# Kernel optimization log

Hardware: AMD Instinct MI355X
Metric: run time of the kernel (lower is better)

## Reference

```python
import jax, jax.numpy as jnp
import numpy as np

B, T, C = 4, 2048, 768
H, D = 12, 64          # num_heads, head_size
R = 64                 # kv_lora_rank
ROPE_THETA = 10000.0


def setup_inputs() -> dict:
    key = jax.random.key(0)
    ks = jax.random.split(key, 8)
    s = lambda fan_in: 1.0 / np.sqrt(fan_in)
    return {
        "x":      jax.random.normal(ks[0], (B, T, C), jnp.float32),
        "Wq":     jax.random.normal(ks[1], (C, H * D), jnp.float32) * s(C),
        "Wdown":  jax.random.normal(ks[2], (C, R), jnp.float32) * s(C),
        "ln_g":   jnp.ones((R,), jnp.float32),
        "ln_b":   jnp.zeros((R,), jnp.float32),
        "Wup":    jax.random.normal(ks[3], (R, 2 * H * D), jnp.float32) * s(R),
        "Wo":     jax.random.normal(ks[4], (H * D, C), jnp.float32) * s(H * D),
        "bo":     jnp.zeros((C,), jnp.float32),
    }


def _rope_cos_sin(t, d, dtype):
    # freqs over half-dim, repeated twice (rotate-half convention)
    inv_freq = 1.0 / (ROPE_THETA ** (jnp.arange(0, d, 2, dtype=jnp.float32) / d))
    ang = jnp.arange(t, dtype=jnp.float32)[:, None] * inv_freq[None, :]  # [T, D/2]
    ang = jnp.concatenate([ang, ang], axis=-1)                            # [T, D]
    return jnp.cos(ang).astype(dtype), jnp.sin(ang).astype(dtype)


def _apply_rope(q, cos, sin):
    # q: [B, H, T, D]; cos/sin: [T, D]
    d2 = q.shape[-1] // 2
    rot = jnp.concatenate([-q[..., d2:], q[..., :d2]], axis=-1)
    return q * cos + rot * sin


def reference(x, Wq, Wdown, ln_g, ln_b, Wup, Wo, bo):
    b, t, c = x.shape
    q = (x @ Wq).reshape(b, t, H, D).transpose(0, 2, 1, 3)  # [B,H,T,D]

    ckv = x @ Wdown                                         # [B,T,R]
    mu = jnp.mean(ckv, axis=-1, keepdims=True)
    var = jnp.var(ckv, axis=-1, keepdims=True)
    ckv = (ckv - mu) * jax.lax.rsqrt(var + 1e-5) * ln_g + ln_b

    kv = (ckv @ Wup).reshape(b, t, 2, H, D)
    k = kv[:, :, 0].transpose(0, 2, 1, 3)                   # [B,H,T,D]
    v = kv[:, :, 1].transpose(0, 2, 1, 3)

    cos, sin = _rope_cos_sin(t, D, x.dtype)
    q = _apply_rope(q, cos, sin)
    k = _apply_rope(k, cos, sin)

    wei = jnp.einsum("bhqd,bhkd->bhqk", q, k) * (D ** -0.5)
    causal = jnp.tril(jnp.ones((t, t), bool))
    wei = jnp.where(causal, wei, -jnp.inf)
    wei = jax.nn.softmax(wei, axis=-1)                      # dropout: eval mode (identity)

    out = jnp.einsum("bhqk,bhkd->bhqd", wei, v)             # [B,H,T,D]
    out = out.transpose(0, 2, 1, 3).reshape(b, t, H * D)
    return out @ Wo + bo
```

## Files before the change

### kernel.cpp

```cpp
#include <hip/hip_runtime.h>
#include <hip/hip_bf16.h>
#include <math.h>

#define B_ 4
#define T_ 2048
#define C_ 768
#define H_ 12
#define D_ 64
#define R_ 64
#define BT_ (B_*T_)
#define HD_ (H_*D_)

typedef __attribute__((ext_vector_type(8))) short bf16x8;
typedef __attribute__((ext_vector_type(4))) float f32x4;
typedef __attribute__((ext_vector_type(16))) float f32x16;

__device__ inline short f2bf(float f) {
  union { float f; unsigned u; } x; x.f = f;
  unsigned r = x.u + 0x7fffu + ((x.u >> 16) & 1u);
  return (short)(r >> 16);
}
__device__ inline unsigned pk_bf16(float a, float b) {
#if __has_builtin(__builtin_amdgcn_cvt_pk_bf16_f32)
  auto t = __builtin_amdgcn_cvt_pk_bf16_f32(a, b);
  unsigned u; __builtin_memcpy(&u, &t, sizeof(unsigned)); return u;
#else
  union { float f; unsigned u; } x, y; x.f = a; y.f = b;
  unsigned ra = (x.u + 0x7fffu + ((x.u >> 16) & 1u)) >> 16;
  unsigned rb = (y.u + 0x7fffu + ((y.u >> 16) & 1u)) & 0xffff0000u;
  return ra | rb;
#endif
}
__device__ inline float fexp2(float x) {
#if __has_builtin(__builtin_amdgcn_exp2f)
  return __builtin_amdgcn_exp2f(x);
#else
  return exp2f(x);
#endif
}
__device__ inline void pswap(unsigned &a, unsigned &b) {
#if __has_builtin(__builtin_amdgcn_permlane32_swap)
  auto r = __builtin_amdgcn_permlane32_swap((int)a, (int)b, false, false);
  unsigned u[2]; __builtin_memcpy(u, &r, 8);
  a = u[0]; b = u[1];
#else
  unsigned ax = __shfl_xor(a, 32), bx = __shfl_xor(b, 32);
  bool hi = (threadIdx.x & 32) != 0;
  unsigned na = hi ? bx : a;
  unsigned nb = hi ? b : ax;
  a = na; b = nb;
#endif
}
typedef __attribute__((address_space(3))) unsigned lds_u32;
typedef __attribute__((address_space(1))) const unsigned glb_u32;
__device__ inline void gload_lds16(const void* g, void* l) {
  __builtin_amdgcn_global_load_lds((glb_u32*)g, (lds_u32*)l, 16, 0, 0);
}

#define SC2_ 0.18033688f

__device__ __attribute__((always_inline)) inline void ttile(
    const float* __restrict__ src, short* __restrict__ dst,
    int Kd, int Ns, int k0, int n0, int tid, float (*tl)[33]) {
  int tx = tid & 31, ty = tid >> 5;
  #pragma unroll
  for (int r = 0; r < 4; ++r)
    tl[ty + 8 * r][tx] = src[(size_t)(k0 + ty + 8 * r) * Ns + n0 + tx];
  __syncthreads();
  #pragma unroll
  for (int r = 0; r < 4; ++r)
    dst[(size_t)(n0 + ty + 8 * r) * Kd + k0 + tx] = f2bf(tl[tx][ty + 8 * r]);
}

__global__ __launch_bounds__(256) void prep_conv(
    const float* __restrict__ Wq, const float* __restrict__ Wd,
    const float* __restrict__ Wup, const float* __restrict__ Wo,
    short* __restrict__ W1T, short* __restrict__ WupT, short* __restrict__ WvoT,
    float* __restrict__ cs, float* __restrict__ sn) {
  __shared__ float SH[32 * 65 + 64 * 33];
  float (*tl)[33] = (float(*)[33])SH;
  int tid = threadIdx.x, blk = blockIdx.x;
  if (blk < 576) {
    int tk = blk % 24, tn = blk / 24;
    ttile(Wq, W1T, 768, 768, tk * 32, tn * 32, tid, tl);
  } else if (blk < 624) {
    int l = blk - 576; int tk = l % 24, tn = l / 24;
    ttile(Wd, W1T + (size_t)768 * 768, 768, 64, tk * 32, tn * 32, tid, tl);
  } else if (blk < 672) {
    int l = blk - 624; int tk = l % 2, tn = l / 2;
    ttile(Wup, WupT, 64, 1536, tk * 32, tn * 32, tid, tl);
  } else if (blk < 1248) {
    int l = blk - 672;
    int h = l / 48, rem = l % 48, tc = rem >> 1, tr = rem & 1;
    float* a  = SH;
    float* bm = SH + 32 * 65;
    #pragma unroll
    for (int i = 0; i < 8; ++i) {
      int idx = tid + i * 256;
      int r = idx >> 6, d = idx & 63;
      a[r * 65 + d] = Wup[(size_t)(tr * 32 + r) * 1536 + 768 + h * 64 + d];
      int dd = idx >> 5, c = idx & 31;
      bm[dd * 33 + c] = Wo[(size_t)(h * 64 + dd) * 768 + tc * 32 + c];
    }
    __syncthreads();
    int r = tid & 31, cj = tid >> 5;
    float s0 = 0.f, s1 = 0.f, s2 = 0.f, s3 = 0.f;
    #pragma unroll
    for (int d = 0; d < 64; ++d) {
      float av = a[r * 65 + d];
      const float* bp = &bm[d * 33 + cj * 4];
      s0 += av * bp[0]; s1 += av * bp[1]; s2 += av * bp[2]; s3 += av * bp[3];
    }
    int colb = tc * 32 + cj * 4;
    size_t krow = (size_t)(h * 64 + tr * 32 + r);
    WvoT[(size_t)(colb + 0) * 768 + krow] = f2bf(s0);
    WvoT[(size_t)(colb + 1) * 768 + krow] = f2bf(s1);
    WvoT[(size_t)(colb + 2) * 768 + krow] = f2bf(s2);
    WvoT[(size_t)(colb + 3) * 768 + krow] = f2bf(s3);
  } else {
    int base = (blk - 1248) * 1024;
    #pragma unroll
    for (int i = 0; i < 4; ++i) {
      int idx = base + tid + i * 256;
      int j = idx & 31, t = idx >> 5;
      float invf = exp2f(-(float)j * (13.287712379549449f / 32.f));
      float ang = (float)t * invf;
      cs[idx] = cosf(ang);
      sn[idx] = sinf(ang);
    }
  }
}

__global__ __launch_bounds__(256) void gemm0_k(
    const float* __restrict__ Af, const short* __restrict__ Bt,
    const float* __restrict__ bias, const float* __restrict__ bias2,
    short* __restrict__ ob0, short* __restrict__ ob1, short* __restrict__ obT,
    const float* __restrict__ cs, const float* __restrict__ sn)
{
  constexpr int K = 768;
  __shared__ short SM[2 * 16384];
  const int m0 = blockIdx.x * 128;
  const int n0 = blockIdx.y * 128;
  const int tid = threadIdx.x, lane = tid & 63, w = tid >> 6;
  const int wr = w >> 1, wc = w & 1;
  const int fr = lane & 15, fk = (lane >> 4) * 8;
  const int rstage = lane >> 3, cstage = (lane & 7) * 8;

  f32x4 acc[4][4] = {};
  auto As = [&](int buf) -> short* { return SM + buf * 16384; };
  auto Bs = [&](int buf) -> short* { return SM + buf * 16384 + 8192; };

  auto compute = [&](const short* Asb, const short* Bsb) {
    #pragma unroll
    for (int kk = 0; kk < 64; kk += 32) {
      bf16x8 a[4], b[4];
      #pragma unroll
      for (int mi = 0; mi < 4; ++mi)
        a[mi] = *(const bf16x8*)&Asb[(wr * 64 + mi * 16 + fr) * 64 + kk + fk];
      #pragma unroll
      for (int ni = 0; ni < 4; ++ni)
        b[ni] = *(const bf16x8*)&Bsb[(wc * 64 + ni * 16 + fr) * 64 + kk + fk];
      #pragma unroll
      for (int mi = 0; mi < 4; ++mi)
        #pragma unroll
        for (int ni = 0; ni < 4; ++ni)
          acc[mi][ni] = __builtin_amdgcn_mfma_f32_16x16x32_bf16(a[mi], b[ni], acc[mi][ni], 0, 0, 0);
    }
  };
  auto stageB = [&](short* Bsb, int k0) {
    #pragma unroll
    for (int i = 0; i < 4; ++i) {
      int c = w * 4 + i;
      int r = c * 8 + rstage;
      gload_lds16(&Bt[(size_t)(n0 + r) * K + k0 + cstage], Bsb + c * 512);
    }
  };

  float4 fa[8];
  auto loadA = [&](int k0) {
    #pragma unroll
    for (int i = 0; i < 4; ++i) {
      int idx = tid + 256 * i;
      int row = idx >> 3, c8 = idx & 7;
      const float* src = Af + (size_t)(m0 + row) * 768 + k0 + c8 * 8;
      fa[2 * i]     = *(const float4*)(src);
      fa[2 * i + 1] = *(const float4*)(src + 4);
    }
  };
  auto writeA = [&](short* Asb) {
    #pragma unroll
    for (int i = 0; i < 4; ++i) {
      int idx = tid + 256 * i;
      int row = idx >> 3, c8 = idx & 7;
      uint4 uu;
      uu.x = pk_bf16(fa[2 * i].x,     fa[2 * i].y);
      uu.y = pk_bf16(fa[2 * i].z,     fa[2 * i].w);
      uu.z = pk_bf16(fa[2 * i + 1].x, fa[2 * i + 1].y);
      uu.w = pk_bf16(fa[2 * i + 1].z, fa[2 * i + 1].w);
      *(uint4*)&Asb[row * 64 + c8 * 8] = uu;
    }
  };

  loadA(0);
  stageB(Bs(0), 0);
  writeA(As(0));
  __syncthreads();

  int buf = 0;
  for (int k0 = 0; k0 < K; k0 += 64) {
    bool nxt = (k0 + 64 < K);
    if (nxt) { loadA(k0 + 64); stageB(Bs(buf ^ 1), k0 + 64); }
    compute(As(buf), Bs(buf));
    if (nxt) writeA(As(buf ^ 1));
    __syncthreads();
    buf ^= 1;
  }

  const int er = (lane >> 4) * 4, ec = lane & 15;
  const int cb = n0 + wc * 64;

  if (cb < 768) {
    int h = cb >> 6;
    #pragma unroll
    for (int mi = 0; mi < 4; ++mi)
      #pragma unroll
      for (int r = 0; r < 4; ++r) {
        int row = m0 + wr * 64 + mi * 16 + er + r;
        int t = row & (T_ - 1), bb = row >> 11;
        short* dst = ob0 + (((size_t)(bb * H_ + h)) * T_ + t) * 64;
        #pragma unroll
        for (int ni = 0; ni < 2; ++ni) {
          int d = ni * 16 + ec;
          float c = cs[t * 32 + d] * SC2_, s = sn[t * 32 + d] * SC2_;
          float x0 = acc[mi][ni][r], x1 = acc[mi][ni + 2][r];
          dst[d]      = f2bf(x0 * c - x1 * s);
          dst[d + 32] = f2bf(x1 * c + x0 * s);
        }
      }
  } else if (cb == 768) {
    short* Wl = SM + w * 2560;
    int bb = m0 >> 11;
    int dl = lane >> 2, tlo = (lane & 3) * 8;
    #pragma unroll
    for (int hp = 0; hp < 2; ++hp) {
      #pragma unroll
      for (int mi2 = 0; mi2 < 2; ++mi2) {
        int mi = hp * 2 + mi2;
        short vb[4][4];
        #pragma unroll
        for (int r = 0; r < 4; ++r) {
          float s = 0.f, s2 = 0.f;
          #pragma unroll
          for (int ni = 0; ni < 4; ++ni) { float v = acc[mi][ni][r]; s += v; s2 += v * v; }
          #pragma unroll
          for (int off = 1; off < 16; off <<= 1) {
            s  += __shfl_xor(s, off);
            s2 += __shfl_xor(s2, off);
          }
          float mu = s * (1.f / 64.f);
          float var = s2 * (1.f / 64.f) - mu * mu;
          float rstd = rsqrtf(var + 1e-5f);
          int row = m0 + wr * 64 + mi * 16 + er + r;
          #pragma unroll
          for (int ni = 0; ni < 4; ++ni) {
            int d = ni * 16 + ec;
            short q = f2bf((acc[mi][ni][r] - mu) * rstd * bias[d] + bias2[d]);
            vb[r][ni] = q;
            ob1[(size_t)row * 64 + d] = q;
          }
        }
        int tl0 = mi2 * 16 + er;
        #pragma unroll
        for (int ni = 0; ni < 4; ++ni) {
          int d = ni * 16 + ec;
          uint2 uu;
          uu.x = (unsigned)(unsigned short)vb[0][ni] | ((unsigned)(unsigned short)vb[1][ni] << 16);
          uu.y = (unsigned)(unsigned short)vb[2][ni] | ((unsigned)(unsigned short)vb[3][ni] << 16);
          *(uint2*)&Wl[d * 40 + tl0] = uu;
        }
      }
      int tg0 = (m0 & (T_ - 1)) + wr * 64 + hp * 32;
      #pragma unroll
      for (int j = 0; j < 4; ++j) {
        int d = j * 16 + dl;
        uint4 vv = *(const uint4*)&Wl[d * 40 + tlo];
        *(uint4*)&obT[((size_t)(bb * 64 + d)) * T_ + tg0 + tlo] = vv;
      }
    }
  }
}

__global__ __launch_bounds__(256) void gemm1_k(
    const short* __restrict__ A, const short* __restrict__ Bt,
    short* __restrict__ ob0,
    const float* __restrict__ cs, const float* __restrict__ sn)
{
  constexpr int K = 64;
  __shared__ short SM[2 * 8192];
  short* As = SM;
  short* Bs = SM + 8192;
  const int m0 = blockIdx.x * 128;
  const int n0 = blockIdx.y * 128;
  const int tid = threadIdx.x, lane = tid & 63, w = tid >> 6;
  const int wr = w >> 1, wc = w & 1;
  const int fr = lane & 15, fk = (lane >> 4) * 8;
  const int rstage = lane >> 3, cstage = (lane & 7) * 8;

  f32x4 acc[4][4] = {};

  #pragma unroll
  for (int i = 0; i < 4; ++i) {
    int c = w * 4 + i;
    int r = c * 8 + rstage;
    gload_lds16(&A[(size_t)(m0 + r) * K + cstage], As + c * 512);
    gload_lds16(&Bt[(size_t)(n0 + r) * K + cstage], Bs + c * 512);
  }
  __syncthreads();
  #pragma unroll
  for (int kk = 0; kk < 64; kk += 32) {
    bf16x8 a[4], b[4];
    #pragma unroll
    for (int mi = 0; mi < 4; ++mi)
      a[mi] = *(const bf16x8*)&As[(wr * 64 + mi * 16 + fr) * 64 + kk + fk];
    #pragma unroll
    for (int ni = 0; ni < 4; ++ni)
      b[ni] = *(const bf16x8*)&Bs[(wc * 64 + ni * 16 + fr) * 64 + kk + fk];
    #pragma unroll
    for (int mi = 0; mi < 4; ++mi)
      #pragma unroll
      for (int ni = 0; ni < 4; ++ni)
        acc[mi][ni] = __builtin_amdgcn_mfma_f32_16x16x32_bf16(a[mi], b[ni], acc[mi][ni], 0, 0, 0);
  }

  const int er = (lane >> 4) * 4, ec = lane & 15;
  const int cb = n0 + wc * 64;
  int h = cb >> 6;
  #pragma unroll
  for (int mi = 0; mi < 4; ++mi)
    #pragma unroll
    for (int r = 0; r < 4; ++r) {
      int row = m0 + wr * 64 + mi * 16 + er + r;
      int t = row & (T_ - 1), bb = row >> 11;
      short* dst = ob0 + (((size_t)(bb * H_ + h)) * T_ + t) * 64;
      #pragma unroll
      for (int ni = 0; ni < 2; ++ni) {
        int d = ni * 16 + ec;
        float c = cs[t * 32 + d], s = sn[t * 32 + d];
        float x0 = acc[mi][ni][r], x1 = acc[mi][ni + 2][r];
        dst[d]      = f2bf(x0 * c - x1 * s);
        dst[d + 32] = f2bf(x1 * c + x0 * s);
      }
    }
}

__global__ __launch_bounds__(256) void attn_mfma(
    const short* __restrict__ qgl, const short* __restrict__ kg,
    const short* __restrict__ vtg, short* __restrict__ o)
{
  __shared__ short SMa[2][2][8 * 512];

  const int bh = blockIdx.x;
  const int u  = 15 - blockIdx.y;
  const int tid = threadIdx.x, lane = tid & 63, w = tid >> 6;
  const int q32 = lane & 31, half = lane >> 5;
  const int b = bh / H_, h = bh - b * H_;
  const short* kb  = kg  + (size_t)bh * T_ * 64;
  const short* vtb = vtg + (size_t)b * 64 * T_;

  const int wq = 4 * u + w;
  const int q0 = wq * 32;
  const int last_w = (wq >> 1) * 64;
  const int qidx = q0 + q32;
  const int kend = (2 * u + 1) * 64;

  const short* qrow = qgl + ((size_t)bh * T_ + qidx) * 64;
  bf16x8 bq[4];
  #pragma unroll
  for (int ks = 0; ks < 4; ++ks)
    bq[ks] = *(const bf16x8*)&qrow[ks * 16 + half * 8];

  f32x16 oacc[2] = {};
  float lrun = 0.f;

  auto stage = [&](int buf, int kt) {
    #pragma unroll
    for (int i = 0; i < 2; ++i) {
      int c = w * 2 + i;
      int kh = c >> 2, ks = c & 3;
      gload_lds16(kb + (size_t)(kt + kh * 32 + q32) * 64 + ks * 16 + half * 8,
                  &SMa[buf][0][c * 512]);
      gload_lds16(vtb + (size_t)(kh * 32 + q32) * T_ + kt + ks * 16 + half * 8,
                  &SMa[buf][1][c * 512]);
    }
  };

  stage(0, 0);
  __syncthreads();

  int cur = 0;
  for (int kt = 0; kt <= kend; kt += 64) {
    if (kt + 64 <= kend) stage(cur ^ 1, kt + 64);

    if (kt <= last_w) {
      const short* Kc = &SMa[cur][0][0];
      const short* Vc = &SMa[cur][1][0];
      const bool diag = (kt == last_w);
      const int dkh = diag ? (wq & 1) : 2;
      const bool skip1 = diag && ((wq & 1) == 0);

      bf16x8 bp[4];
      #pragma unroll
      for (int kh = 0; kh < 2; ++kh) {
        if (kh == 1 && skip1) break;
        f32x16 sacc = {};
        __builtin_amdgcn_s_setprio(1);
        #pragma unroll
        for (int ks = 0; ks < 4; ++ks) {
          bf16x8 a = *(const bf16x8*)&Kc[(kh * 4 + ks) * 512 + lane * 8];
          sacc = __builtin_amdgcn_mfma_f32_32x32x16_bf16(a, bq[ks], sacc, 0, 0, 0);
        }
        __builtin_amdgcn_s_setprio(0);
        float pv[16];
        if (kh != dkh) {
          #pragma unroll
          for (int r = 0; r < 16; ++r) pv[r] = fexp2(sacc[r]);
        } else {
          #pragma unroll
          for (int r = 0; r < 16; ++r) {
            int key = kt + kh * 32 + (r & 3) + 8 * (r >> 2) + 4 * half;
            pv[r] = (key <= qidx) ? fexp2(sacc[r]) : 0.f;
          }
        }
        float t0 = (pv[0] + pv[1]) + (pv[2] + pv[3]);
        float t1 = (pv[4] + pv[5]) + (pv[6] + pv[7]);
        float t2 = (pv[8] + pv[9]) + (pv[10] + pv[11]);
        float t3 = (pv[12] + pv[13]) + (pv[14] + pv[15]);
        lrun += (t0 + t1) + (t2 + t3);
        unsigned l0 = pk_bf16(pv[0],  pv[1]),  h0 = pk_bf16(pv[2],  pv[3]);
        unsigned l1 = pk_bf16(pv[4],  pv[5]),  h1 = pk_bf16(pv[6],  pv[7]);
        unsigned l2 = pk_bf16(pv[8],  pv[9]),  h2 = pk_bf16(pv[10], pv[11]);
        unsigned l3 = pk_bf16(pv[12], pv[13]), h3 = pk_bf16(pv[14], pv[15]);
        pswap(l0, l1); pswap(h0, h1);
        pswap(l2, l3); pswap(h2, h3);
        union { unsigned u[4]; bf16x8 v; } f0, f1;
        f0.u[0] = l0; f0.u[1] = h0; f0.u[2] = l1; f0.u[3] = h1;
        f1.u[0] = l2; f1.u[1] = h2; f1.u[2] = l3; f1.u[3] = h3;
        bp[2 * kh + 0] = f0.v;
        bp[2 * kh + 1] = f1.v;
      }

      __builtin_amdgcn_s_setprio(1);
      #pragma unroll
      for (int ks = 0; ks < 2; ++ks)
        #pragma unroll
        for (int dt = 0; dt < 2; ++dt) {
          bf16x8 av = *(const bf16x8*)&Vc[(dt * 4 + ks) * 512 + lane * 8];
          oacc[dt] = __builtin_amdgcn_mfma_f32_32x32x16_bf16(av, bp[ks], oacc[dt], 0, 0, 0);
        }
      if (!skip1) {
        #pragma unroll
        for (int ks = 2; ks < 4; ++ks)
          #pragma unroll
          for (int dt = 0; dt < 2; ++dt) {
            bf16x8 av = *(const bf16x8*)&Vc[(dt * 4 + ks) * 512 + lane * 8];
            oacc[dt] = __builtin_amdgcn_mfma_f32_32x32x16_bf16(av, bp[ks], oacc[dt], 0, 0, 0);
          }
      }
      __builtin_amdgcn_s_setprio(0);
    }

    __syncthreads();
    cur ^= 1;
  }

  float ltot = lrun + __shfl_xor(lrun, 32);
  float inv = 1.f / ltot;
  short* Pw = &SMa[0][0][0] + w * 2304;
  #pragma unroll
  for (int dt = 0; dt < 2; ++dt)
    #pragma unroll
    for (int g2 = 0; g2 < 4; ++g2) {
      uint2 uu;
      uu.x = pk_bf16(oacc[dt][4 * g2 + 0] * inv, oacc[dt][4 * g2 + 1] * inv);
      uu.y = pk_bf16(oacc[dt][4 * g2 + 2] * inv, oacc[dt][4 * g2 + 3] * inv);
      *(uint2*)&Pw[q32 * 72 + dt * 32 + 8 * g2 + 4 * half] = uu;
    }
  int row = lane >> 1, seg = lane & 1;
  int t = q0 + row;
  short* orow = o + ((size_t)(b * T_ + t)) * HD_ + h * 64 + seg * 32;
  #pragma unroll
  for (int i = 0; i < 4; ++i) {
    uint4 vv = *(const uint4*)&Pw[row * 72 + seg * 32 + i * 8];
    *(uint4*)&orow[i * 8] = vv;
  }
}

__global__ __launch_bounds__(256) void gemm_out(
    const short* __restrict__ A, const short* __restrict__ Bt,
    float* __restrict__ out0, const float* __restrict__ bias)
{
  constexpr int K = HD_, N = C_;
  __shared__ short SM[2 * (8192 + 4096)];
  const int m0 = blockIdx.x * 128;
  const int n0 = blockIdx.y * 64;
  const int tid = threadIdx.x, lane = tid & 63, w = tid >> 6;
  const int fr = lane & 15, fk = (lane >> 4) * 8;
  const int rstage = lane >> 3, cstage = (lane & 7) * 8;

  f32x4 acc[2][4] = {};

  auto As = [&](int buf) -> short* { return SM + buf * 12288; };
  auto Bs = [&](int buf) -> short* { return SM + buf * 12288 + 8192; };

  auto stage = [&](int buf, int k0) {
    #pragma unroll
    for (int i = 0; i < 4; ++i) {
      int c = w * 4 + i;
      int r = c * 8 + rstage;
      gload_lds16(&A[(size_t)(m0 + r) * K + k0 + cstage], As(buf) + c * 512);
    }
    #pragma unroll
    for (int i = 0; i < 2; ++i) {
      int c = w * 2 + i;
      int r = c * 8 + rstage;
      gload_lds16(&Bt[(size_t)(n0 + r) * K + k0 + cstage], Bs(buf) + c * 512);
    }
  };

  stage(0, 0);
  __syncthreads();

  int buf = 0;
  for (int k0 = 0; k0 < K; k0 += 64) {
    if (k0 + 64 < K) stage(buf ^ 1, k0 + 64);
    #pragma unroll
    for (int kk = 0; kk < 64; kk += 32) {
      bf16x8 a[2], b[4];
      a[0] = *(const bf16x8*)&As(buf)[(w * 32 +      fr) * 64 + kk + fk];
      a[1] = *(const bf16x8*)&As(buf)[(w * 32 + 16 + fr) * 64 + kk + fk];
      #pragma unroll
      for (int ni = 0; ni < 4; ++ni)
        b[ni] = *(const bf16x8*)&Bs(buf)[(ni * 16 + fr) * 64 + kk + fk];
      #pragma unroll
      for (int mi = 0; mi < 2; ++mi)
        #pragma unroll
        for (int ni = 0; ni < 4; ++ni)
          acc[mi][ni] = __builtin_amdgcn_mfma_f32_16x16x32_bf16(a[mi], b[ni], acc[mi][ni], 0, 0, 0);
    }
    __syncthreads();
    buf ^= 1;
  }

  const int er = (lane >> 4) * 4, ec = lane & 15;
  #pragma unroll
  for (int mi = 0; mi < 2; ++mi)
    #pragma unroll
    for (int r = 0; r < 4; ++r) {
      int row = m0 + w * 32 + mi * 16 + er + r;
      #pragma unroll
      for (int ni = 0; ni < 4; ++ni) {
        int col = n0 + ni * 16 + ec;
        out0[(size_t)row * N + col] = acc[mi][ni][r] + bias[col];
      }
    }
}

extern "C" void kernel_launch(void* const* d_in, const int* in_sizes, int n_in,
                              void* d_out, int out_size, void* d_ws, size_t ws_size,
                              hipStream_t stream) {
  (void)in_sizes; (void)n_in; (void)out_size; (void)ws_size;
  const float* x     = (const float*)d_in[0];
  const float* Wq    = (const float*)d_in[1];
  const float* Wdown = (const float*)d_in[2];
  const float* ln_g  = (const float*)d_in[3];
  const float* ln_b  = (const float*)d_in[4];
  const float* Wup   = (const float*)d_in[5];
  const float* Wo    = (const float*)d_in[6];
  const float* bo    = (const float*)d_in[7];
  float* out = (float*)d_out;

  char* w = (char*)d_ws;
  short* W1T    = (short*)w;  w += (size_t)896 * C_    * 2;
  short* WupT   = (short*)w;  w += (size_t)HD_ * R_    * 2;
  short* WvoT   = (short*)w;  w += (size_t)C_ * HD_    * 2;
  short* ckv    = (short*)w;  w += (size_t)BT_ * R_    * 2;
  short* ckvT   = (short*)w;  w += (size_t)B_ * R_ * T_ * 2;
  short* qb     = (short*)w;  w += (size_t)BT_ * HD_   * 2;
  short* kb     = (short*)w;  w += (size_t)BT_ * HD_   * 2;
  short* att    = (short*)w;  w += (size_t)BT_ * HD_   * 2;
  float* cs_t   = (float*)w;  w += (size_t)T_ * 32 * 4;
  float* sn_t   = (float*)w;  w += (size_t)T_ * 32 * 4;

  prep_conv<<<1312, 256, 0, stream>>>(Wq, Wdown, Wup, Wo,
                                      W1T, WupT, WvoT, cs_t, sn_t);

  gemm0_k<<<dim3(BT_/128, 7), 256, 0, stream>>>(
      x, W1T, ln_g, ln_b, qb, ckv, ckvT, cs_t, sn_t);

  gemm1_k<<<dim3(BT_/128, 6), 256, 0, stream>>>(
      ckv, WupT, kb, cs_t, sn_t);

  attn_mfma<<<dim3(B_*H_, 16), 256, 0, stream>>>(qb, kb, ckvT, att);

  gemm_out<<<dim3(BT_/128, 12), 256, 0, stream>>>(att, WvoT, out, bo);
}
```

Measured before the change: 195.7 us.

## Fuse K up-projection with RoPE into latent-panel blocks of first GEMM

Removes the separate gemm1 kernel. The blocks that compute the normalized latent ckv now keep it in LDS and immediately multiply it by WupT across six double-buffered 128-column chunks, applying RoPE and writing K directly. The ckv global round trip and one kernel launch go away. Those blocks are remapped to blockIdx.y==0 so they are scheduled first, which offsets their much longer runtime. The cost is a serialized extra tail inside 64 blocks, which may lengthen the critical path of the fused kernel.

```diff
diff --git a/kernel.cpp b/kernel.cpp
--- a/kernel.cpp
+++ b/kernel.cpp
@@ -133,14 +133,16 @@
 
 __global__ __launch_bounds__(256) void gemm0_k(
     const float* __restrict__ Af, const short* __restrict__ Bt,
+    const short* __restrict__ WupT,
     const float* __restrict__ bias, const float* __restrict__ bias2,
-    short* __restrict__ ob0, short* __restrict__ ob1, short* __restrict__ obT,
+    short* __restrict__ ob0, short* __restrict__ obT, short* __restrict__ kb_o,
     const float* __restrict__ cs, const float* __restrict__ sn)
 {
   constexpr int K = 768;
   __shared__ short SM[2 * 16384];
+  const int panel = (blockIdx.y == 0) ? 6 : (int)blockIdx.y - 1;
   const int m0 = blockIdx.x * 128;
-  const int n0 = blockIdx.y * 128;
+  const int n0 = panel * 128;
   const int tid = threadIdx.x, lane = tid & 63, w = tid >> 6;
   const int wr = w >> 1, wc = w & 1;
   const int fr = lane & 15, fk = (lane >> 4) * 8;
@@ -238,7 +240,7 @@
         }
       }
   } else if (cb == 768) {
-    short* Wl = SM + w * 2560;
+    short* Wl = SM + 16384 + w * 2560;
     int bb = m0 >> 11;
     int dl = lane >> 2, tlo = (lane & 3) * 8;
     #pragma unroll
@@ -260,13 +262,13 @@
           float mu = s * (1.f / 64.f);
           float var = s2 * (1.f / 64.f) - mu * mu;
           float rstd = rsqrtf(var + 1e-5f);
-          int row = m0 + wr * 64 + mi * 16 + er + r;
+          int lr = wr * 64 + mi * 16 + er + r;
           #pragma unroll
           for (int ni = 0; ni < 4; ++ni) {
             int d = ni * 16 + ec;
             short q = f2bf((acc[mi][ni][r] - mu) * rstd * bias[d] + bias2[d]);
             vb[r][ni] = q;
-            ob1[(size_t)row * 64 + d] = q;
+            SM[lr * 64 + d] = q;
           }
         }
         int tl0 = mi2 * 16 + er;
@@ -288,69 +290,62 @@
       }
     }
   }
-}
-
-__global__ __launch_bounds__(256) void gemm1_k(
-    const short* __restrict__ A, const short* __restrict__ Bt,
-    short* __restrict__ ob0,
-    const float* __restrict__ cs, const float* __restrict__ sn)
-{
-  constexpr int K = 64;
-  __shared__ short SM[2 * 8192];
-  short* As = SM;
-  short* Bs = SM + 8192;
-  const int m0 = blockIdx.x * 128;
-  const int n0 = blockIdx.y * 128;
-  const int tid = threadIdx.x, lane = tid & 63, w = tid >> 6;
-  const int wr = w >> 1, wc = w & 1;
-  const int fr = lane & 15, fk = (lane >> 4) * 8;
-  const int rstage = lane >> 3, cstage = (lane & 7) * 8;
-
-  f32x4 acc[4][4] = {};
-
-  #pragma unroll
-  for (int i = 0; i < 4; ++i) {
-    int c = w * 4 + i;
-    int r = c * 8 + rstage;
-    gload_lds16(&A[(size_t)(m0 + r) * K + cstage], As + c * 512);
-    gload_lds16(&Bt[(size_t)(n0 + r) * K + cstage], Bs + c * 512);
-  }
-  __syncthreads();
-  #pragma unroll
-  for (int kk = 0; kk < 64; kk += 32) {
-    bf16x8 a[4], b[4];
-    #pragma unroll
-    for (int mi = 0; mi < 4; ++mi)
-      a[mi] = *(const bf16x8*)&As[(wr * 64 + mi * 16 + fr) * 64 + kk + fk];
-    #pragma unroll
-    for (int ni = 0; ni < 4; ++ni)
-      b[ni] = *(const bf16x8*)&Bs[(wc * 64 + ni * 16 + fr) * 64 + kk + fk];
-    #pragma unroll
-    for (int mi = 0; mi < 4; ++mi)
-      #pragma unroll
-      for (int ni = 0; ni < 4; ++ni)
-        acc[mi][ni] = __builtin_amdgcn_mfma_f32_16x16x32_bf16(a[mi], b[ni], acc[mi][ni], 0, 0, 0);
-  }
-
-  const int er = (lane >> 4) * 4, ec = lane & 15;
-  const int cb = n0 + wc * 64;
-  int h = cb >> 6;
-  #pragma unroll
-  for (int mi = 0; mi < 4; ++mi)
-    #pragma unroll
-    for (int r = 0; r < 4; ++r) {
-      int row = m0 + wr * 64 + mi * 16 + er + r;
-      int t = row & (T_ - 1), bb = row >> 11;
-      short* dst = ob0 + (((size_t)(bb * H_ + h)) * T_ + t) * 64;
-      #pragma unroll
-      for (int ni = 0; ni < 2; ++ni) {
-        int d = ni * 16 + ec;
-        float c = cs[t * 32 + d], s = sn[t * 32 + d];
-        float x0 = acc[mi][ni][r], x1 = acc[mi][ni + 2][r];
-        dst[d]      = f2bf(x0 * c - x1 * s);
-        dst[d + 32] = f2bf(x1 * c + x0 * s);
-      }
-    }
+
+  if (panel == 6) {
+    short* Bk0 = SM + 8192;
+    short* Bk1 = SM + 24576;
+    auto stageBk = [&](short* Bsb, int c) {
+      #pragma unroll
+      for (int i = 0; i < 4; ++i) {
+        int cc = w * 4 + i;
+        int r = cc * 8 + rstage;
+        gload_lds16(&WupT[(size_t)(c * 128 + r) * 64 + cstage], Bsb + cc * 512);
+      }
+    };
+    stageBk(Bk0, 0);
+    __syncthreads();
+
+    int bku = 0;
+    for (int c = 0; c < 6; ++c) {
+      if (c < 5) stageBk(bku ? Bk0 : Bk1, c + 1);
+      const short* Bc = bku ? Bk1 : Bk0;
+      f32x4 kacc[4][4] = {};
+      #pragma unroll
+      for (int kk = 0; kk < 64; kk += 32) {
+        bf16x8 a[4], b[4];
+        #pragma unroll
+        for (int mi = 0; mi < 4; ++mi)
+          a[mi] = *(const bf16x8*)&SM[(wr * 64 + mi * 16 + fr) * 64 + kk + fk];
+        #pragma unroll
+        for (int ni = 0; ni < 4; ++ni)
+          b[ni] = *(const bf16x8*)&Bc[(wc * 64 + ni * 16 + fr) * 64 + kk + fk];
+        #pragma unroll
+        for (int mi = 0; mi < 4; ++mi)
+          #pragma unroll
+          for (int ni = 0; ni < 4; ++ni)
+            kacc[mi][ni] = __builtin_amdgcn_mfma_f32_16x16x32_bf16(a[mi], b[ni], kacc[mi][ni], 0, 0, 0);
+      }
+      int hk = c * 2 + wc;
+      #pragma unroll
+      for (int mi = 0; mi < 4; ++mi)
+        #pragma unroll
+        for (int r = 0; r < 4; ++r) {
+          int row = m0 + wr * 64 + mi * 16 + er + r;
+          int t = row & (T_ - 1), bb = row >> 11;
+          short* dst = kb_o + (((size_t)(bb * H_ + hk)) * T_ + t) * 64;
+          #pragma unroll
+          for (int ni = 0; ni < 2; ++ni) {
+            int d = ni * 16 + ec;
+            float cc = cs[t * 32 + d], ss = sn[t * 32 + d];
+            float x0 = kacc[mi][ni][r], x1 = kacc[mi][ni + 2][r];
+            dst[d]      = f2bf(x0 * cc - x1 * ss);
+            dst[d + 32] = f2bf(x1 * cc + x0 * ss);
+          }
+        }
+      __syncthreads();
+      bku ^= 1;
+    }
+  }
 }
 
 __global__ __launch_bounds__(256) void attn_mfma(
@@ -583,7 +578,6 @@
   short* W1T    = (short*)w;  w += (size_t)896 * C_    * 2;
   short* WupT   = (short*)w;  w += (size_t)HD_ * R_    * 2;
   short* WvoT   = (short*)w;  w += (size_t)C_ * HD_    * 2;
-  short* ckv    = (short*)w;  w += (size_t)BT_ * R_    * 2;
   short* ckvT   = (short*)w;  w += (size_t)B_ * R_ * T_ * 2;
   short* qb     = (short*)w;  w += (size_t)BT_ * HD_   * 2;
   short* kb     = (short*)w;  w += (size_t)BT_ * HD_   * 2;
@@ -595,10 +589,7 @@
                                       W1T, WupT, WvoT, cs_t, sn_t);
 
   gemm0_k<<<dim3(BT_/128, 7), 256, 0, stream>>>(
-      x, W1T, ln_g, ln_b, qb, ckv, ckvT, cs_t, sn_t);
-
-  gemm1_k<<<dim3(BT_/128, 6), 256, 0, stream>>>(
-      ckv, WupT, kb, cs_t, sn_t);
+      x, W1T, WupT, ln_g, ln_b, qb, ckvT, kb, cs_t, sn_t);
 
   attn_mfma<<<dim3(B_*H_, 16), 256, 0, stream>>>(qb, kb, ckvT, att);
 
```

Result: slower. 205.4 us (+5.0%).

## Split attention KV range across two waves per query tile and merge partials

Applied to the files above, without the earlier changes.

The attention kernel moves from 256 to 512 threads. Each 32-row query tile is now handled by two waves, each covering half of the causal key range. The second wave writes its unnormalized output accumulator and row sum to LDS, and the first wave adds them in before normalizing and storing. This gives more parallelism and shortens the per-wave critical path. In exchange it adds an LDS reduction, another barrier and higher register and occupancy pressure per block. Staging loads are spread across all 8 waves.

```diff
diff --git a/kernel.cpp b/kernel.cpp
--- a/kernel.cpp
+++ b/kernel.cpp
@@ -353,31 +353,37 @@
     }
 }
 
-__global__ __launch_bounds__(256) void attn_mfma(
+__global__ __launch_bounds__(512) void attn_mfma(
     const short* __restrict__ qgl, const short* __restrict__ kg,
     const short* __restrict__ vtg, short* __restrict__ o)
 {
   __shared__ short SMa[2][2][8 * 512];
+  __shared__ float lex[4][64];
 
   const int bh = blockIdx.x;
-  const int u  = 15 - blockIdx.y;
+  const int j  = 15 - blockIdx.y;
   const int tid = threadIdx.x, lane = tid & 63, w = tid >> 6;
-  const int q32 = lane & 31, half = lane >> 5;
+  const int q32 = lane & 31, hl = lane >> 5;
   const int b = bh / H_, h = bh - b * H_;
   const short* kb  = kg  + (size_t)bh * T_ * 64;
   const short* vtb = vtg + (size_t)b * 64 * T_;
 
-  const int wq = 4 * u + w;
+  const int wq = 4 * j + (w >> 1);
+  const int halfw = w & 1;
   const int q0 = wq * 32;
-  const int last_w = (wq >> 1) * 64;
   const int qidx = q0 + q32;
-  const int kend = (2 * u + 1) * 64;
+  const int nt = (wq >> 1) + 1;
+  const int hsp = (nt + 1) >> 1;
+  const int myks = halfw ? hsp * 64 : 0;
+  const int myke = (halfw ? nt : hsp) * 64;
+  const int dgk = (wq >> 1) * 64;
+  const int kend = (2 * j + 1) * 64;
 
   const short* qrow = qgl + ((size_t)bh * T_ + qidx) * 64;
   bf16x8 bq[4];
   #pragma unroll
   for (int ks = 0; ks < 4; ++ks)
-    bq[ks] = *(const bf16x8*)&qrow[ks * 16 + half * 8];
+    bq[ks] = *(const bf16x8*)&qrow[ks * 16 + hl * 8];
 
   f32x16 oacc[2] = {};
   float lrun = 0.f;
@@ -386,11 +392,14 @@
     #pragma unroll
     for (int i = 0; i < 2; ++i) {
       int c = w * 2 + i;
-      int kh = c >> 2, ks = c & 3;
-      gload_lds16(kb + (size_t)(kt + kh * 32 + q32) * 64 + ks * 16 + half * 8,
-                  &SMa[buf][0][c * 512]);
-      gload_lds16(vtb + (size_t)(kh * 32 + q32) * T_ + kt + ks * 16 + half * 8,
-                  &SMa[buf][1][c * 512]);
+      if (c < 8) {
+        gload_lds16(kb + (size_t)(kt + (c >> 2) * 32 + q32) * 64 + (c & 3) * 16 + hl * 8,
+                    &SMa[buf][0][c * 512]);
+      } else {
+        int cv = c - 8;
+        gload_lds16(vtb + (size_t)((cv >> 2) * 32 + q32) * T_ + kt + (cv & 3) * 16 + hl * 8,
+                    &SMa[buf][1][cv * 512]);
+      }
     }
   };
 
@@ -401,10 +410,10 @@
   for (int kt = 0; kt <= kend; kt += 64) {
     if (kt + 64 <= kend) stage(cur ^ 1, kt + 64);
 
-    if (kt <= last_w) {
+    if (kt >= myks && kt < myke) {
       const short* Kc = &SMa[cur][0][0];
       const short* Vc = &SMa[cur][1][0];
-      const bool diag = (kt == last_w);
+      const bool diag = (kt == dgk);
       const int dkh = diag ? (wq & 1) : 2;
       const bool skip1 = diag && ((wq & 1) == 0);
 
@@ -427,7 +436,7 @@
         } else {
           #pragma unroll
           for (int r = 0; r < 16; ++r) {
-            int key = kt + kh * 32 + (r & 3) + 8 * (r >> 2) + 4 * half;
+            int key = kt + kh * 32 + (r & 3) + 8 * (r >> 2) + 4 * hl;
             pv[r] = (key <= qidx) ? fexp2(sacc[r]) : 0.f;
           }
         }
@@ -473,25 +482,44 @@
     cur ^= 1;
   }
 
-  float ltot = lrun + __shfl_xor(lrun, 32);
-  float inv = 1.f / ltot;
-  short* Pw = &SMa[0][0][0] + w * 2304;
-  #pragma unroll
-  for (int dt = 0; dt < 2; ++dt)
-    #pragma unroll
-    for (int g2 = 0; g2 < 4; ++g2) {
-      uint2 uu;
-      uu.x = pk_bf16(oacc[dt][4 * g2 + 0] * inv, oacc[dt][4 * g2 + 1] * inv);
-      uu.y = pk_bf16(oacc[dt][4 * g2 + 2] * inv, oacc[dt][4 * g2 + 3] * inv);
-      *(uint2*)&Pw[q32 * 72 + dt * 32 + 8 * g2 + 4 * half] = uu;
-    }
-  int row = lane >> 1, seg = lane & 1;
-  int t = q0 + row;
-  short* orow = o + ((size_t)(b * T_ + t)) * HD_ + h * 64 + seg * 32;
-  #pragma unroll
-  for (int i = 0; i < 4; ++i) {
-    uint4 vv = *(const uint4*)&Pw[row * 72 + seg * 32 + i * 8];
-    *(uint4*)&orow[i * 8] = vv;
+  const int pidx = w >> 1;
+  float* ex = (float*)&SMa[0][0][0] + pidx * 2048;
+  if (halfw) {
+    #pragma unroll
+    for (int dt = 0; dt < 2; ++dt)
+      #pragma unroll
+      for (int r = 0; r < 16; ++r)
+        ex[(dt * 16 + r) * 64 + lane] = oacc[dt][r];
+    lex[pidx][lane] = lrun;
+  }
+  __syncthreads();
+  if (!halfw) {
+    #pragma unroll
+    for (int dt = 0; dt < 2; ++dt)
+      #pragma unroll
+      for (int r = 0; r < 16; ++r)
+        oacc[dt][r] += ex[(dt * 16 + r) * 64 + lane];
+    lrun += lex[pidx][lane];
+    float ltot = lrun + __shfl_xor(lrun, 32);
+    float inv = 1.f / ltot;
+    short* Pw = (short*)ex;
+    #pragma unroll
+    for (int dt = 0; dt < 2; ++dt)
+      #pragma unroll
+      for (int g2 = 0; g2 < 4; ++g2) {
+        uint2 uu;
+        uu.x = pk_bf16(oacc[dt][4 * g2 + 0] * inv, oacc[dt][4 * g2 + 1] * inv);
+        uu.y = pk_bf16(oacc[dt][4 * g2 + 2] * inv, oacc[dt][4 * g2 + 3] * inv);
+        *(uint2*)&Pw[q32 * 72 + dt * 32 + 8 * g2 + 4 * hl] = uu;
+      }
+    int row = lane >> 1, seg = lane & 1;
+    int t = q0 + row;
+    short* orow = o + ((size_t)(b * T_ + t)) * HD_ + h * 64 + seg * 32;
+    #pragma unroll
+    for (int i = 0; i < 4; ++i) {
+      uint4 vv = *(const uint4*)&Pw[row * 72 + seg * 32 + i * 8];
+      *(uint4*)&orow[i * 8] = vv;
+    }
   }
 }
 
@@ -600,7 +628,7 @@
   gemm1_k<<<dim3(BT_/128, 6), 256, 0, stream>>>(
       ckv, WupT, kb, cs_t, sn_t);
 
-  attn_mfma<<<dim3(B_*H_, 16), 256, 0, stream>>>(qb, kb, ckvT, att);
+  attn_mfma<<<dim3(B_*H_, 16), 512, 0, stream>>>(qb, kb, ckvT, att);
 
   gemm_out<<<dim3(BT_/128, 12), 256, 0, stream>>>(att, WvoT, out, bo);
 }
```

After: 203.5 us. +4.0%, slower.
